# Kernel tuning notes

Hardware: AMD Instinct MI355X
Metric: run time of the kernel (lower is better)

The kernel has to match this reference:

```python
import jax, jax.numpy as jnp
import numpy as np

N = 50000   # num nodes
E = 600000  # num edges per signed adjacency
D = 128     # feature dim
K = 10      # num_diff_layers
C = 0.15    # restart probability


def setup_inputs() -> dict:
    key = jax.random.key(0)
    ks = jax.random.split(key, 8)
    rows_p = jax.random.randint(ks[0], (E,), 0, N, dtype=jnp.int32)
    cols_p = jax.random.randint(ks[1], (E,), 0, N, dtype=jnp.int32)
    vals_p = jax.random.uniform(ks[2], (E,), dtype=jnp.float32)
    rows_m = jax.random.randint(ks[3], (E,), 0, N, dtype=jnp.int32)
    cols_m = jax.random.randint(ks[4], (E,), 0, N, dtype=jnp.int32)
    vals_m = jax.random.uniform(ks[5], (E,), dtype=jnp.float32)
    X = jax.random.normal(ks[6], (N, D), dtype=jnp.float32)
    # torch code draws old_M ~ Uniform(-1, 1) at forward time; we expose it as input
    M0 = jax.random.uniform(ks[7], (N, D), dtype=jnp.float32, minval=-1.0, maxval=1.0)
    return {"rows_p": rows_p, "cols_p": cols_p, "vals_p": vals_p,
            "rows_m": rows_m, "cols_m": cols_m, "vals_m": vals_m,
            "X": X, "M0": M0}


def _spmm(rows, cols, vals, dense):
    # COO sparse [N,N] @ dense [N,D]: gather columns, scale, scatter-add to rows
    return jax.ops.segment_sum(vals[:, None] * dense[cols], rows,
                               num_segments=dense.shape[0])


def reference(rows_p, cols_p, vals_p, rows_m, cols_m, vals_m, X, M0):
    tilda_X = C * X  # restart term
    P, M = X, M0
    for _ in range(K):
        new_P = _spmm(rows_p, cols_p, vals_p, P) + _spmm(rows_m, cols_m, vals_m, M) + tilda_X
        new_M = _spmm(rows_m, cols_m, vals_m, P) + _spmm(rows_p, cols_p, vals_p, M)
        P, M = new_P, new_M
    return (P, M)
```

## Files before the change

### kernel.cpp

```cpp
#include <hip/hip_runtime.h>
#include <math.h>


#define TB 256

__device__ __forceinline__ unsigned pack_bf16(float a, float b) {
    unsigned ua = __float_as_uint(a), ub = __float_as_uint(b);
    ua += 0x7fffu + ((ua >> 16) & 1u);
    ub += 0x7fffu + ((ub >> 16) & 1u);
    return (ua >> 16) | (ub & 0xffff0000u);
}

__device__ __forceinline__ float2 unpack_bf16(unsigned w) {
    float2 r;
    r.x = __uint_as_float(w << 16);
    r.y = __uint_as_float(w & 0xffff0000u);
    return r;
}

__global__ void zero_int_kernel(int* __restrict__ p, int n) {
    int i = blockIdx.x * blockDim.x + threadIdx.x;
    if (i < n) p[i] = 0;
}

__global__ void bucket_count_kernel(const int* __restrict__ rows_p,
                                    const int* __restrict__ rows_m,
                                    int E, int* __restrict__ bcnt) {
    __shared__ int h[128];
    for (int i = threadIdx.x; i < 128; i += TB) h[i] = 0;
    __syncthreads();
    int total = 2 * E;
    for (int e = blockIdx.x * TB + threadIdx.x; e < total; e += gridDim.x * TB) {
        int r = (e < E) ? rows_p[e] : rows_m[e - E];
        atomicAdd(&h[r >> 9], 1);
    }
    __syncthreads();
    for (int i = threadIdx.x; i < 128; i += TB)
        if (h[i]) atomicAdd(&bcnt[i], h[i]);
}

__global__ void bucket_scan_kernel(const int* __restrict__ bcnt,
                                   int* __restrict__ boff, int* __restrict__ bcur) {
    int l = threadIdx.x;
    int v0 = bcnt[l], v1 = bcnt[l + 64];
    int i0 = v0, i1 = v1;
#pragma unroll
    for (int o = 1; o < 64; o <<= 1) { int y = __shfl_up(i0, o); if (l >= o) i0 += y; }
#pragma unroll
    for (int o = 1; o < 64; o <<= 1) { int y = __shfl_up(i1, o); if (l >= o) i1 += y; }
    int t0 = __shfl(i0, 63);
    int e0 = i0 - v0;
    int e1 = i1 - v1 + t0;
    boff[l] = e0;      boff[l + 64] = e1;
    bcur[l] = e0;      bcur[l + 64] = e1;
    if (l == 63) boff[128] = i1 + t0;
}

__global__ __launch_bounds__(TB) void partition_kernel(
    const int* __restrict__ rows_p, const int* __restrict__ cols_p,
    const float* __restrict__ vals_p,
    const int* __restrict__ rows_m, const int* __restrict__ cols_m,
    const float* __restrict__ vals_m, int E,
    int* __restrict__ bcur_g, uint2* __restrict__ stage) {
    __shared__ unsigned keys[2048];
    __shared__ float    vals[2048];
    __shared__ unsigned skeys[2048];
    __shared__ float    svals[2048];
    __shared__ int h[128], boff[128], bcur[128], bbase[128];
    int tile0 = blockIdx.x * 2048;
    int cnt = min(2048, 2 * E - tile0);

    for (int i = threadIdx.x; i < cnt; i += TB) {
        int e = tile0 + i; int r, c; float v;
        if (e < E) { r = rows_p[e]; c = cols_p[e]; v = vals_p[e]; }
        else       { r = rows_m[e - E]; c = cols_m[e - E]; v = -vals_m[e - E]; }
        keys[i] = ((unsigned)r << 16) | (unsigned)c;
        vals[i] = v;
    }
    for (int i = threadIdx.x; i < 128; i += TB) { h[i] = 0; bcur[i] = 0; }
    __syncthreads();
    for (int i = threadIdx.x; i < cnt; i += TB) atomicAdd(&h[keys[i] >> 25], 1);
    __syncthreads();
    if (threadIdx.x < 64) {
        int l = threadIdx.x;
        int v0 = h[l], v1 = h[l + 64], i0 = v0, i1 = v1;
#pragma unroll
        for (int o = 1; o < 64; o <<= 1) { int y = __shfl_up(i0, o); if (l >= o) i0 += y; }
#pragma unroll
        for (int o = 1; o < 64; o <<= 1) { int y = __shfl_up(i1, o); if (l >= o) i1 += y; }
        int t0 = __shfl(i0, 63);
        boff[l] = i0 - v0;
        boff[l + 64] = i1 - v1 + t0;
    }
    __syncthreads();
    for (int i = threadIdx.x; i < cnt; i += TB) {
        unsigned k = keys[i]; int b = k >> 25;
        int p = boff[b] + atomicAdd(&bcur[b], 1);
        skeys[p] = k; svals[p] = vals[i];
    }
    __syncthreads();
    if (threadIdx.x < 128) {
        int c_ = h[threadIdx.x];
        if (c_) bbase[threadIdx.x] = atomicAdd(&bcur_g[threadIdx.x], c_);
    }
    __syncthreads();
    for (int i = threadIdx.x; i < cnt; i += TB) {
        unsigned k = skeys[i]; int b = k >> 25;
        stage[bbase[b] + (i - boff[b])] = make_uint2(k, __float_as_uint(svals[i]));
    }
}

__global__ __launch_bounds__(TB) void csr_finalize_kernel(
    const uint2* __restrict__ stage, const int* __restrict__ boff_g,
    int NBv, int N, int E2, int* __restrict__ off, int2* __restrict__ edge) {
    __shared__ int rc[512], ro[512], rcur[512];
    int b = blockIdx.x;
    int row0 = b << 9;
    int s0 = boff_g[b], s1 = boff_g[b + 1];
    for (int i = threadIdx.x; i < 512; i += TB) { rc[i] = 0; rcur[i] = 0; }
    __syncthreads();
    for (int i = s0 + threadIdx.x; i < s1; i += TB)
        atomicAdd(&rc[(stage[i].x >> 16) - row0], 1);
    __syncthreads();
    if (threadIdx.x < 64) {
        int l = threadIdx.x;
        int s = 0, loc[8];
#pragma unroll
        for (int j = 0; j < 8; ++j) { loc[j] = s; s += rc[l * 8 + j]; }
        int incl = s;
#pragma unroll
        for (int o = 1; o < 64; o <<= 1) { int y = __shfl_up(incl, o); if (l >= o) incl += y; }
        int base = incl - s;
#pragma unroll
        for (int j = 0; j < 8; ++j) ro[l * 8 + j] = base + loc[j];
    }
    __syncthreads();
    for (int i = threadIdx.x; i < 512; i += TB) {
        int r = row0 + i;
        if (r < N) off[r] = s0 + ro[i];
    }
    if (b == NBv - 1 && threadIdx.x == 0) off[N] = E2;
    for (int i = s0 + threadIdx.x; i < s1; i += TB) {
        uint2 rec = stage[i];
        int lr = (int)(rec.x >> 16) - row0;
        int p = s0 + ro[lr] + atomicAdd(&rcur[lr], 1);
        edge[p] = make_int2((int)(rec.x & 0xffffu), (int)rec.y);
    }
}

__global__ void init_kernel(const float* __restrict__ X, const float* __restrict__ M0,
                            uint2* __restrict__ SD, uint2* __restrict__ tXb, int n32) {
    int i = blockIdx.x * blockDim.x + threadIdx.x;
    if (i < n32) {
        int r = i >> 5, q = i & 31;
        float4 x = ((const float4*)X)[(size_t)r * 32 + q];
        float4 m = ((const float4*)M0)[(size_t)r * 32 + q];
        SD[(size_t)r * 64 + q]      = make_uint2(pack_bf16(x.x + m.x, x.y + m.y),
                                                 pack_bf16(x.z + m.z, x.w + m.w));
        SD[(size_t)r * 64 + 32 + q] = make_uint2(pack_bf16(x.x - m.x, x.y - m.y),
                                                 pack_bf16(x.z - m.z, x.w - m.w));
        tXb[(size_t)r * 32 + q]     = make_uint2(pack_bf16(0.15f * x.x, 0.15f * x.y),
                                                 pack_bf16(0.15f * x.z, 0.15f * x.w));
    }
}

__global__ __launch_bounds__(TB) void layer_kernel(
    const int* __restrict__ off, const int2* __restrict__ edge,
    const uint2* __restrict__ In, uint2* __restrict__ Out,
    const uint2* __restrict__ tXb,
    float* __restrict__ Pout, float* __restrict__ Mout, int last, int N) {
    int row = blockIdx.x * 4 + (threadIdx.x >> 6);
    if (row >= N) return;
    int lane = threadIdx.x & 63;
    int sel = lane >> 5;
    int q = lane & 31;

    uint2 t = tXb[(size_t)row * 32 + q];
    float2 t0 = unpack_bf16(t.x), t1 = unpack_bf16(t.y);
    float a0 = t0.x, a1 = t0.y, a2 = t1.x, a3 = t1.y;

    int bg = off[row], e = off[row + 1];
    int j = bg;
    for (; j + 8 <= e; j += 8) {
        int2 e0 = edge[j],     e1 = edge[j + 1], e2 = edge[j + 2], e3 = edge[j + 3];
        int2 e4 = edge[j + 4], e5 = edge[j + 5], e6 = edge[j + 6], e7 = edge[j + 7];
        uint2 w0 = In[(size_t)e0.x * 64 + lane];
        uint2 w1 = In[(size_t)e1.x * 64 + lane];
        uint2 w2 = In[(size_t)e2.x * 64 + lane];
        uint2 w3 = In[(size_t)e3.x * 64 + lane];
        uint2 w4 = In[(size_t)e4.x * 64 + lane];
        uint2 w5 = In[(size_t)e5.x * 64 + lane];
        uint2 w6 = In[(size_t)e6.x * 64 + lane];
        uint2 w7 = In[(size_t)e7.x * 64 + lane];
        float v0 = __int_as_float(e0.y), v1 = __int_as_float(e1.y);
        float v2 = __int_as_float(e2.y), v3 = __int_as_float(e3.y);
        float v4 = __int_as_float(e4.y), v5 = __int_as_float(e5.y);
        float v6 = __int_as_float(e6.y), v7 = __int_as_float(e7.y);
        if (!sel) {
            v0 = fabsf(v0); v1 = fabsf(v1); v2 = fabsf(v2); v3 = fabsf(v3);
            v4 = fabsf(v4); v5 = fabsf(v5); v6 = fabsf(v6); v7 = fabsf(v7);
        }
        float2 g0a = unpack_bf16(w0.x), g0b = unpack_bf16(w0.y);
        float2 g1a = unpack_bf16(w1.x), g1b = unpack_bf16(w1.y);
        float2 g2a = unpack_bf16(w2.x), g2b = unpack_bf16(w2.y);
        float2 g3a = unpack_bf16(w3.x), g3b = unpack_bf16(w3.y);
        float2 g4a = unpack_bf16(w4.x), g4b = unpack_bf16(w4.y);
        float2 g5a = unpack_bf16(w5.x), g5b = unpack_bf16(w5.y);
        float2 g6a = unpack_bf16(w6.x), g6b = unpack_bf16(w6.y);
        float2 g7a = unpack_bf16(w7.x), g7b = unpack_bf16(w7.y);
        a0 += v0 * g0a.x + v1 * g1a.x + v2 * g2a.x + v3 * g3a.x
            + v4 * g4a.x + v5 * g5a.x + v6 * g6a.x + v7 * g7a.x;
        a1 += v0 * g0a.y + v1 * g1a.y + v2 * g2a.y + v3 * g3a.y
            + v4 * g4a.y + v5 * g5a.y + v6 * g6a.y + v7 * g7a.y;
        a2 += v0 * g0b.x + v1 * g1b.x + v2 * g2b.x + v3 * g3b.x
            + v4 * g4b.x + v5 * g5b.x + v6 * g6b.x + v7 * g7b.x;
        a3 += v0 * g0b.y + v1 * g1b.y + v2 * g2b.y + v3 * g3b.y
            + v4 * g4b.y + v5 * g5b.y + v6 * g6b.y + v7 * g7b.y;
    }
    for (; j < e; ++j) {
        int2 ed = edge[j];
        uint2 w = In[(size_t)ed.x * 64 + lane];
        float v = __int_as_float(ed.y);
        if (!sel) v = fabsf(v);
        float2 ga = unpack_bf16(w.x), gb = unpack_bf16(w.y);
        a0 += v * ga.x; a1 += v * ga.y; a2 += v * gb.x; a3 += v * gb.y;
    }

    if (!last) {
        Out[(size_t)row * 64 + lane] = make_uint2(pack_bf16(a0, a1), pack_bf16(a2, a3));
    } else {
        float b0 = __shfl_xor(a0, 32), b1 = __shfl_xor(a1, 32);
        float b2 = __shfl_xor(a2, 32), b3 = __shfl_xor(a3, 32);
        if (sel == 0) {
            ((float4*)Pout)[(size_t)row * 32 + q] =
                make_float4(0.5f * (a0 + b0), 0.5f * (a1 + b1),
                            0.5f * (a2 + b2), 0.5f * (a3 + b3));
        } else {
            ((float4*)Mout)[(size_t)row * 32 + q] =
                make_float4(0.5f * (b0 - a0), 0.5f * (b1 - a1),
                            0.5f * (b2 - a2), 0.5f * (b3 - a3));
        }
    }
}

extern "C" void kernel_launch(void* const* d_in, const int* in_sizes, int n_in,
                              void* d_out, int out_size, void* d_ws, size_t ws_size,
                              hipStream_t stream) {
    const int*   rows_p = (const int*)d_in[0];
    const int*   cols_p = (const int*)d_in[1];
    const float* vals_p = (const float*)d_in[2];
    const int*   rows_m = (const int*)d_in[3];
    const int*   cols_m = (const int*)d_in[4];
    const float* vals_m = (const float*)d_in[5];
    const float* X      = (const float*)d_in[6];
    const float* M0     = (const float*)d_in[7];

    const int E = in_sizes[0];
    const int D = 128;
    const int N = in_sizes[6] / D;
    const int K = 10;
    const int E2 = 2 * E;
    const size_t ND = (size_t)N * D;
    const int N32 = N * 32;
    const int NBv = (N + 511) >> 9;

    float* outP = (float*)d_out;
    float* outM = outP + ND;

    char* ws = (char*)d_ws;
    size_t o = 0;
    auto alloc = [&](size_t b) -> void* {
        void* p = ws + o;
        o += (b + 255) & ~(size_t)255;
        return p;
    };
    uint2* SDA  = (uint2*)alloc((size_t)N * 64 * 8);
    uint2* SDB  = (uint2*)alloc((size_t)N * 64 * 8);
    uint2* tXb  = (uint2*)alloc((size_t)N * 32 * 8);
    int*   off  = (int*)alloc((size_t)(N + 1) * sizeof(int));
    int2*  edge = (int2*)alloc((size_t)E2 * sizeof(int2));
    int*   bcnt = (int*)alloc(128 * sizeof(int));
    int*   boff = (int*)alloc(129 * sizeof(int));
    int*   bcur = (int*)alloc(128 * sizeof(int));
    uint2* stage = SDB;

    int gN32 = (N32 + TB - 1) / TB;
    int gTiles = (E2 + 2047) / 2048;

    zero_int_kernel<<<1, 128, 0, stream>>>(bcnt, 128);
    bucket_count_kernel<<<512, TB, 0, stream>>>(rows_p, rows_m, E, bcnt);
    bucket_scan_kernel<<<1, 64, 0, stream>>>(bcnt, boff, bcur);
    partition_kernel<<<gTiles, TB, 0, stream>>>(rows_p, cols_p, vals_p,
                                                rows_m, cols_m, vals_m, E,
                                                bcur, stage);
    csr_finalize_kernel<<<NBv, TB, 0, stream>>>(stage, boff, NBv, N, E2, off, edge);

    init_kernel<<<gN32, TB, 0, stream>>>(X, M0, SDA, tXb, N32);

    int gL = (N + 3) / 4;
    uint2 *Si = SDA, *So = SDB;
    for (int k = 0; k < K; ++k) {
        int last = (k == K - 1);
        layer_kernel<<<gL, TB, 0, stream>>>(off, edge, Si, So, tXb,
                                            outP, outM, last, N);
        uint2* t = Si; Si = So; So = t;
    }
}
```

Measured before the change: 1.007 ms.

## Split feature dim into column chunks with per-chunk layout and edge-parallel lanes

The combined P+M / P-M bf16 state is re-laid out as 8 column chunks, each stored contiguously per row as 64 bytes, and every layer block handles one chunk for 16 rows. Within a wavefront, 8 edges are gathered in parallel by lane groups and then reduced with shuffles. The goal is a gather footprint per pass that fits in cache and more memory-level parallelism per row. The cost is more edge-list reads (once per chunk), extra shuffle reductions, and only 8 of 64 lanes doing the stores.

```diff
diff --git a/kernel.cpp b/kernel.cpp
--- a/kernel.cpp
+++ b/kernel.cpp
@@ -149,18 +149,21 @@
 }
 
 __global__ void init_kernel(const float* __restrict__ X, const float* __restrict__ M0,
-                            uint2* __restrict__ SD, uint2* __restrict__ tXb, int n32) {
+                            uint2* __restrict__ SD, uint2* __restrict__ tXb,
+                            int n32, int N) {
     int i = blockIdx.x * blockDim.x + threadIdx.x;
     if (i < n32) {
-        int r = i >> 5, q = i & 31;
-        float4 x = ((const float4*)X)[(size_t)r * 32 + q];
-        float4 m = ((const float4*)M0)[(size_t)r * 32 + q];
-        SD[(size_t)r * 64 + q]      = make_uint2(pack_bf16(x.x + m.x, x.y + m.y),
-                                                 pack_bf16(x.z + m.z, x.w + m.w));
-        SD[(size_t)r * 64 + 32 + q] = make_uint2(pack_bf16(x.x - m.x, x.y - m.y),
-                                                 pack_bf16(x.z - m.z, x.w - m.w));
-        tXb[(size_t)r * 32 + q]     = make_uint2(pack_bf16(0.15f * x.x, 0.15f * x.y),
-                                                 pack_bf16(0.15f * x.z, 0.15f * x.w));
+        int r = i >> 5, q5 = i & 31;
+        int c = q5 >> 2, q = q5 & 3;
+        float4 x = ((const float4*)X)[(size_t)r * 32 + q5];
+        float4 m = ((const float4*)M0)[(size_t)r * 32 + q5];
+        size_t rb = (size_t)c * N + r;
+        SD[rb * 8 + q]     = make_uint2(pack_bf16(x.x + m.x, x.y + m.y),
+                                        pack_bf16(x.z + m.z, x.w + m.w));
+        SD[rb * 8 + 4 + q] = make_uint2(pack_bf16(x.x - m.x, x.y - m.y),
+                                        pack_bf16(x.z - m.z, x.w - m.w));
+        tXb[rb * 4 + q]    = make_uint2(pack_bf16(0.15f * x.x, 0.15f * x.y),
+                                        pack_bf16(0.15f * x.z, 0.15f * x.w));
     }
 }
 
@@ -169,76 +172,79 @@
     const uint2* __restrict__ In, uint2* __restrict__ Out,
     const uint2* __restrict__ tXb,
     float* __restrict__ Pout, float* __restrict__ Mout, int last, int N) {
-    int row = blockIdx.x * 4 + (threadIdx.x >> 6);
-    if (row >= N) return;
+    int c = blockIdx.x & 7;
+    int rowblk = blockIdx.x >> 3;
+    int wid = threadIdx.x >> 6;
     int lane = threadIdx.x & 63;
-    int sel = lane >> 5;
-    int q = lane & 31;
-
-    uint2 t = tXb[(size_t)row * 32 + q];
-    float2 t0 = unpack_bf16(t.x), t1 = unpack_bf16(t.y);
-    float a0 = t0.x, a1 = t0.y, a2 = t1.x, a3 = t1.y;
-
-    int bg = off[row], e = off[row + 1];
-    int j = bg;
-    for (; j + 8 <= e; j += 8) {
-        int2 e0 = edge[j],     e1 = edge[j + 1], e2 = edge[j + 2], e3 = edge[j + 3];
-        int2 e4 = edge[j + 4], e5 = edge[j + 5], e6 = edge[j + 6], e7 = edge[j + 7];
-        uint2 w0 = In[(size_t)e0.x * 64 + lane];
-        uint2 w1 = In[(size_t)e1.x * 64 + lane];
-        uint2 w2 = In[(size_t)e2.x * 64 + lane];
-        uint2 w3 = In[(size_t)e3.x * 64 + lane];
-        uint2 w4 = In[(size_t)e4.x * 64 + lane];
-        uint2 w5 = In[(size_t)e5.x * 64 + lane];
-        uint2 w6 = In[(size_t)e6.x * 64 + lane];
-        uint2 w7 = In[(size_t)e7.x * 64 + lane];
-        float v0 = __int_as_float(e0.y), v1 = __int_as_float(e1.y);
-        float v2 = __int_as_float(e2.y), v3 = __int_as_float(e3.y);
-        float v4 = __int_as_float(e4.y), v5 = __int_as_float(e5.y);
-        float v6 = __int_as_float(e6.y), v7 = __int_as_float(e7.y);
-        if (!sel) {
-            v0 = fabsf(v0); v1 = fabsf(v1); v2 = fabsf(v2); v3 = fabsf(v3);
-            v4 = fabsf(v4); v5 = fabsf(v5); v6 = fabsf(v6); v7 = fabsf(v7);
+    int slot = lane & 7;
+    int e_sub = lane >> 3;
+    int sys = slot >> 2;
+    int q = slot & 3;
+    unsigned vmask = sys ? 0xffffffffu : 0x7fffffffu;
+
+    const uint2* Inc  = In  + (size_t)c * N * 8;
+    uint2*       Outc = Out + (size_t)c * N * 8;
+    const uint2* tXc  = tXb + (size_t)c * N * 4;
+
+    int row0 = (rowblk << 4) + (wid << 2);
+    for (int rr = 0; rr < 4; ++rr) {
+        int row = row0 + rr;
+        if (row >= N) return;
+        int bg = off[row], en = off[row + 1];
+        float a0 = 0.f, a1 = 0.f, a2 = 0.f, a3 = 0.f;
+
+        int j = bg;
+        for (; j + 16 <= en; j += 16) {
+            int2 eA = edge[j + e_sub];
+            int2 eB = edge[j + 8 + e_sub];
+            uint2 wA = Inc[(size_t)eA.x * 8 + slot];
+            uint2 wB = Inc[(size_t)eB.x * 8 + slot];
+            float vA = __uint_as_float(((unsigned)eA.y) & vmask);
+            float vB = __uint_as_float(((unsigned)eB.y) & vmask);
+            float2 gA0 = unpack_bf16(wA.x), gA1 = unpack_bf16(wA.y);
+            float2 gB0 = unpack_bf16(wB.x), gB1 = unpack_bf16(wB.y);
+            a0 += vA * gA0.x + vB * gB0.x;
+            a1 += vA * gA0.y + vB * gB0.y;
+            a2 += vA * gA1.x + vB * gB1.x;
+            a3 += vA * gA1.y + vB * gB1.y;
         }
-        float2 g0a = unpack_bf16(w0.x), g0b = unpack_bf16(w0.y);
-        float2 g1a = unpack_bf16(w1.x), g1b = unpack_bf16(w1.y);
-        float2 g2a = unpack_bf16(w2.x), g2b = unpack_bf16(w2.y);
-        float2 g3a = unpack_bf16(w3.x), g3b = unpack_bf16(w3.y);
-        float2 g4a = unpack_bf16(w4.x), g4b = unpack_bf16(w4.y);
-        float2 g5a = unpack_bf16(w5.x), g5b = unpack_bf16(w5.y);
-        float2 g6a = unpack_bf16(w6.x), g6b = unpack_bf16(w6.y);
-        float2 g7a = unpack_bf16(w7.x), g7b = unpack_bf16(w7.y);
-        a0 += v0 * g0a.x + v1 * g1a.x + v2 * g2a.x + v3 * g3a.x
-            + v4 * g4a.x + v5 * g5a.x + v6 * g6a.x + v7 * g7a.x;
-        a1 += v0 * g0a.y + v1 * g1a.y + v2 * g2a.y + v3 * g3a.y
-            + v4 * g4a.y + v5 * g5a.y + v6 * g6a.y + v7 * g7a.y;
-        a2 += v0 * g0b.x + v1 * g1b.x + v2 * g2b.x + v3 * g3b.x
-            + v4 * g4b.x + v5 * g5b.x + v6 * g6b.x + v7 * g7b.x;
-        a3 += v0 * g0b.y + v1 * g1b.y + v2 * g2b.y + v3 * g3b.y
-            + v4 * g4b.y + v5 * g5b.y + v6 * g6b.y + v7 * g7b.y;
-    }
-    for (; j < e; ++j) {
-        int2 ed = edge[j];
-        uint2 w = In[(size_t)ed.x * 64 + lane];
-        float v = __int_as_float(ed.y);
-        if (!sel) v = fabsf(v);
-        float2 ga = unpack_bf16(w.x), gb = unpack_bf16(w.y);
-        a0 += v * ga.x; a1 += v * ga.y; a2 += v * gb.x; a3 += v * gb.y;
-    }
-
-    if (!last) {
-        Out[(size_t)row * 64 + lane] = make_uint2(pack_bf16(a0, a1), pack_bf16(a2, a3));
-    } else {
-        float b0 = __shfl_xor(a0, 32), b1 = __shfl_xor(a1, 32);
-        float b2 = __shfl_xor(a2, 32), b3 = __shfl_xor(a3, 32);
-        if (sel == 0) {
-            ((float4*)Pout)[(size_t)row * 32 + q] =
-                make_float4(0.5f * (a0 + b0), 0.5f * (a1 + b1),
-                            0.5f * (a2 + b2), 0.5f * (a3 + b3));
+        for (; j < en; j += 8) {
+            int idx = j + e_sub;
+            int2 er = make_int2(0, 0);
+            if (idx < en) er = edge[idx];
+            uint2 w = Inc[(size_t)er.x * 8 + slot];
+            float v = __uint_as_float(((unsigned)er.y) & vmask);
+            float2 g0 = unpack_bf16(w.x), g1 = unpack_bf16(w.y);
+            a0 += v * g0.x; a1 += v * g0.y; a2 += v * g1.x; a3 += v * g1.y;
+        }
+
+        a0 += __shfl_xor(a0, 8); a0 += __shfl_xor(a0, 16); a0 += __shfl_xor(a0, 32);
+        a1 += __shfl_xor(a1, 8); a1 += __shfl_xor(a1, 16); a1 += __shfl_xor(a1, 32);
+        a2 += __shfl_xor(a2, 8); a2 += __shfl_xor(a2, 16); a2 += __shfl_xor(a2, 32);
+        a3 += __shfl_xor(a3, 8); a3 += __shfl_xor(a3, 16); a3 += __shfl_xor(a3, 32);
+
+        uint2 t = tXc[(size_t)row * 4 + q];
+        float2 t0 = unpack_bf16(t.x), t1 = unpack_bf16(t.y);
+        a0 += t0.x; a1 += t0.y; a2 += t1.x; a3 += t1.y;
+
+        if (!last) {
+            if (lane < 8)
+                Outc[(size_t)row * 8 + slot] =
+                    make_uint2(pack_bf16(a0, a1), pack_bf16(a2, a3));
         } else {
-            ((float4*)Mout)[(size_t)row * 32 + q] =
-                make_float4(0.5f * (b0 - a0), 0.5f * (b1 - a1),
-                            0.5f * (b2 - a2), 0.5f * (b3 - a3));
+            float b0 = __shfl_xor(a0, 4), b1 = __shfl_xor(a1, 4);
+            float b2 = __shfl_xor(a2, 4), b3 = __shfl_xor(a3, 4);
+            if (lane < 8) {
+                if (sys == 0) {
+                    ((float4*)Pout)[(size_t)row * 32 + 4 * c + q] =
+                        make_float4(0.5f * (a0 + b0), 0.5f * (a1 + b1),
+                                    0.5f * (a2 + b2), 0.5f * (a3 + b3));
+                } else {
+                    ((float4*)Mout)[(size_t)row * 32 + 4 * c + q] =
+                        make_float4(0.5f * (b0 - a0), 0.5f * (b1 - a1),
+                                    0.5f * (b2 - a2), 0.5f * (b3 - a3));
+                }
+            }
         }
     }
 }
@@ -295,9 +301,10 @@
                                                 bcur, stage);
     csr_finalize_kernel<<<NBv, TB, 0, stream>>>(stage, boff, NBv, N, E2, off, edge);
 
-    init_kernel<<<gN32, TB, 0, stream>>>(X, M0, SDA, tXb, N32);
-
-    int gL = (N + 3) / 4;
+    init_kernel<<<gN32, TB, 0, stream>>>(X, M0, SDA, tXb, N32, N);
+
+    int nRB = (N + 15) >> 4;
+    int gL = nRB * 8;
     uint2 *Si = SDA, *So = SDB;
     for (int k = 0; k < K; ++k) {
         int last = (k == K - 1);
```

Result: slower. 1.528 ms (+51.8%).
